# Kernel optimization log

Measured on AMD Instinct MI355X. Metric: run time of the kernel, lower is better.

The kernel has to match this reference:

```python
import jax, jax.numpy as jnp
import numpy as np

N = 100000          # num nodes
E = 1600000         # num edges (before self loops)
IN_C = 128
OUT_C = 64
RATIO = 0.5
NEG_SLOPE = 0.2


def setup_inputs() -> dict:
    key = jax.random.key(0)
    k1, k2, k3, k4, k5 = jax.random.split(key, 5)
    x = jax.random.normal(k1, (N, IN_C), jnp.float32)
    # edges with no self loops (module removes then re-adds self loops)
    src = jax.random.randint(k2, (E,), 0, N, dtype=jnp.int32)
    off = jax.random.randint(k3, (E,), 1, N, dtype=jnp.int32)
    tgt = (src + off) % N
    edge_index = jnp.stack([src, tgt])  # [2, E], row0=source(j), row1=target(i)
    # glorot init
    s_w = float(np.sqrt(6.0 / (IN_C + OUT_C)))
    weight = jax.random.uniform(k4, (IN_C, OUT_C), jnp.float32, -s_w, s_w)
    s_a = float(np.sqrt(6.0 / (1 + 2 * OUT_C)))
    att = jax.random.uniform(k5, (1, 2 * OUT_C), jnp.float32, -s_a, s_a)
    batch = jnp.zeros((N,), jnp.int32)  # single graph
    return {"x": x, "weight": weight, "att": att,
            "edge_index": edge_index, "batch": batch, "bn": 0}


def reference(x, weight, att, edge_index, batch, bn):
    # add self loops (static shapes: E + N edges)
    loops = jnp.arange(N, dtype=edge_index.dtype)
    src = jnp.concatenate([edge_index[0], loops])  # edge_index_j (source)
    tgt = jnp.concatenate([edge_index[1], loops])  # edge_index_i (target)

    h = x @ weight                      # [N, OUT_C]
    x_j = h[src]                        # [E+N, OUT_C] gathered source feats
    x_i = h[tgt]

    # alpha = (cat([x_i, x_j]) * att).sum(-1)
    alpha = x_i @ att[0, :OUT_C] + x_j @ att[0, OUT_C:]   # [E+N]
    alpha = jnp.where(alpha > 0, alpha, NEG_SLOPE * alpha)  # leaky_relu

    # edge-softmax grouped by target node (every node has a self loop -> no empty segment)
    m = jax.ops.segment_max(alpha, tgt, num_segments=N)
    a = jnp.exp(alpha - m[tgt])
    denom = jax.ops.segment_sum(a, tgt, num_segments=N)
    alpha = a / (denom[tgt] + 1e-16)

    # node importance = sum of attention over outgoing edges (grouped by source)
    alpha_sum = jax.ops.segment_sum(alpha, src, num_segments=N)

    # topk node selection (ratio of all nodes; single graph)
    k = int(np.ceil(RATIO * N))
    _, topk_idx = jax.lax.top_k(alpha_sum, k)
    node_mask = jnp.zeros((N,), bool).at[topk_idx].set(True)

    # filter_dn: keep edges whose both endpoints survive; mask instead of compacting
    edge_mask = node_mask[src] & node_mask[tgt]
    alpha_m = jnp.where(edge_mask, alpha, 0.0)

    # weighted scatter-add aggregation to target nodes (aggr='add')
    out = jax.ops.segment_sum(alpha_m[:, None] * x_j, tgt, num_segments=N)  # [N, OUT_C]
    # bn flag is 0 -> BatchNorm skipped
    return out, edge_mask, node_mask
```

## Files before the change

### kernel.cpp

```cpp
#include <hip/hip_runtime.h>
#include <stdint.h>

#define IN_C 128
#define OUT_C 64
#define NEG_SLOPE 0.2f
#define RB 256
#define RBINS 512
#define STAGE 8192
#define SCAP 5120
#define SGRID (RBINS * SCAP)
#define KC 8
#define SXW 192

typedef unsigned int u32;
typedef unsigned char u8;
typedef unsigned long long u64;

__device__ __forceinline__ u32 fenc(float f) {
  u32 u = __float_as_uint(f);
  return (u & 0x80000000u) ? ~u : (u | 0x80000000u);
}
__device__ __forceinline__ u64 key64(float v, int i) {
  return (((u64)fenc(v)) << 32) | (u64)(0xffffffffu - (u32)i);
}

__global__ __launch_bounds__(128) void k_gemm(const float* __restrict__ x,
                                              const float* __restrict__ w,
                                              const float* __restrict__ att,
                                              float* __restrict__ h,
                                              float* __restrict__ ai, float* __restrict__ aj,
                                              int N) {
  __shared__ float sw[IN_C * OUT_C];
  __shared__ float sx[KC * SXW];
  int tid = threadIdx.x;
  int rbase = blockIdx.x * 128;

  for (int i = tid; i < (IN_C * OUT_C) / 4; i += 128)
    ((float4*)sw)[i] = ((const float4*)w)[i];

  int c0 = (tid & 7) * 8;
  int rg = tid >> 3;
  int sxbase = rg * 12;
  float acc[8][8];
#pragma unroll
  for (int i = 0; i < 8; i++)
#pragma unroll
    for (int j = 0; j < 8; j++) acc[i][j] = 0.f;

  int grow = rbase + tid;
  int base = (tid >> 3) * 12 + (tid & 7);
  const float* xp = &x[(size_t)grow * IN_C];

  float4 pv0 = make_float4(0.f, 0.f, 0.f, 0.f);
  float4 pv1 = make_float4(0.f, 0.f, 0.f, 0.f);
  if (grow < N) {
    pv0 = *(const float4*)&xp[0];
    pv1 = *(const float4*)&xp[4];
  }

  for (int kb = 0; kb < IN_C; kb += KC) {
    __syncthreads();
    sx[0 * SXW + base] = pv0.x;
    sx[1 * SXW + base] = pv0.y;
    sx[2 * SXW + base] = pv0.z;
    sx[3 * SXW + base] = pv0.w;
    sx[4 * SXW + base] = pv1.x;
    sx[5 * SXW + base] = pv1.y;
    sx[6 * SXW + base] = pv1.z;
    sx[7 * SXW + base] = pv1.w;
    if (kb + KC < IN_C && grow < N) {
      pv0 = *(const float4*)&xp[kb + KC];
      pv1 = *(const float4*)&xp[kb + KC + 4];
    }
    __syncthreads();
#pragma unroll
    for (int kl = 0; kl < KC; ++kl) {
      int kg = kb + kl;
      float xr[8], wv[8];
      *(float4*)&xr[0] = *(const float4*)&sx[kl * SXW + sxbase];
      *(float4*)&xr[4] = *(const float4*)&sx[kl * SXW + sxbase + 4];
      *(float4*)&wv[0] = *(const float4*)&sw[kg * OUT_C + c0];
      *(float4*)&wv[4] = *(const float4*)&sw[kg * OUT_C + c0 + 4];
#pragma unroll
      for (int i = 0; i < 8; ++i)
#pragma unroll
        for (int j = 0; j < 8; ++j)
          acc[i][j] += xr[i] * wv[j];
    }
  }

  float pi[8], pj[8];
#pragma unroll
  for (int i = 0; i < 8; ++i) { pi[i] = 0.f; pj[i] = 0.f; }
#pragma unroll
  for (int j = 0; j < 8; ++j) {
    float a0 = att[c0 + j], a1 = att[OUT_C + c0 + j];
#pragma unroll
    for (int i = 0; i < 8; ++i) {
      pi[i] += acc[i][j] * a0;
      pj[i] += acc[i][j] * a1;
    }
  }
#pragma unroll
  for (int o = 1; o < 8; o <<= 1) {
#pragma unroll
    for (int i = 0; i < 8; ++i) {
      pi[i] += __shfl_xor(pi[i], o);
      pj[i] += __shfl_xor(pj[i], o);
    }
  }
#pragma unroll
  for (int i = 0; i < 8; ++i) {
    int row = rbase + rg * 8 + i;
    if (row < N) {
      *(float4*)&h[(size_t)row * OUT_C + c0]     = make_float4(acc[i][0], acc[i][1], acc[i][2], acc[i][3]);
      *(float4*)&h[(size_t)row * OUT_C + c0 + 4] = make_float4(acc[i][4], acc[i][5], acc[i][6], acc[i][7]);
      if ((tid & 7) == 0) { ai[row] = pi[i]; aj[row] = pj[i]; }
    }
  }
}

__global__ __launch_bounds__(256) void k_part_t(const int* __restrict__ src, const int* __restrict__ tgt,
                                                int E, int EN, int chunk,
                                                u32* __restrict__ gcurT, u32* __restrict__ bufS,
                                                u32* __restrict__ sel, u32 kSel) {
  __shared__ u32 lh[RBINS];
  __shared__ u32 cur[RBINS];
  int tid = threadIdx.x, b = blockIdx.x;
  if (b == 0 && tid == 0) { sel[0] = 0u; sel[1] = 0u; sel[2] = kSel; sel[3] = 0u; }
  for (int d = tid; d < RBINS; d += 256) lh[d] = 0u;
  __syncthreads();
  int lo = b * chunk, hi = min(lo + chunk, EN);
  for (int e = lo + tid; e < hi; e += 256) {
    int t = (e < E) ? tgt[e] : e - E;
    atomicAdd(&lh[((u32)t) >> 8], 1u);
  }
  __syncthreads();
  for (int d = tid; d < RBINS; d += 256) {
    u32 c = lh[d];
    cur[d] = c ? (u32)(d * SCAP) + atomicAdd(&gcurT[d], c) : 0u;
  }
  __syncthreads();
  for (int e = lo + tid; e < hi; e += 256) {
    int s, t;
    if (e < E) { s = src[e]; t = tgt[e]; } else { s = t = e - E; }
    u32 tb = ((u32)t) >> 8;
    u32 p = atomicAdd(&cur[tb], 1u);
    if (p < (tb + 1u) * SCAP) bufS[p] = (((u32)t & 255u) << 24) | (u32)s;
  }
}

__global__ __launch_bounds__(256) void k_rpass2(const u32* __restrict__ in, u32* __restrict__ out,
                                                const u32* __restrict__ gcurT, u32* __restrict__ gcurS,
                                                u32* __restrict__ offT,
                                                const float* __restrict__ ai, const float* __restrict__ aj,
                                                float* __restrict__ alpha,
                                                u8* __restrict__ pidx, float* __restrict__ pval,
                                                int N) {
  __shared__ u32 hist[256];
  __shared__ u32 sc[256];
  __shared__ u32 lhs[RBINS];
  __shared__ u32 stage[STAGE];
  int tid = threadIdx.x, d = blockIdx.x;
  u32 start = (u32)(d * SCAP);
  u32 cntb = min(gcurT[d], (u32)SCAP);
  u32 end = start + cntb;
  int sz = (int)cntb;
  hist[tid] = 0u;
  for (int dd = tid; dd < RBINS; dd += 256) lhs[dd] = 0u;
  __syncthreads();
  for (u32 p = start + tid; p < end; p += 256) {
    u32 it = in[p];
    atomicAdd(&hist[it >> 24], 1u);
    atomicAdd(&lhs[(it & 0xffffffu) >> 8], 1u);
  }
  __syncthreads();
  for (int dd = tid; dd < RBINS; dd += 256) {
    u32 c = lhs[dd];
    lhs[dd] = c ? (u32)(dd * SCAP) + atomicAdd(&gcurS[dd], c) : 0u;
  }
  u32 hv = hist[tid];
  sc[tid] = hv;
  __syncthreads();
  for (int o = 1; o < 256; o <<= 1) {
    u32 t = (tid >= o) ? sc[tid - o] : 0u;
    __syncthreads();
    sc[tid] += t;
    __syncthreads();
  }
  u32 excl = sc[tid] - hv;
  int node = (d << 8) + tid;
  if (node < N) offT[node] = start + excl;
  if (node == N - 1) offT[N] = start + sc[tid];
  hist[tid] = excl;
  __syncthreads();
  bool staged = (sz <= STAGE);
  for (u32 p = start + tid; p < end; p += 256) {
    u32 it = in[p];
    u32 lp = atomicAdd(&hist[it >> 24], 1u);
    if (staged) stage[lp] = it;
    else out[start + lp] = it;
  }
  __syncthreads();
  if (staged)
    for (int i = tid; i < sz; i += 256) out[start + i] = stage[i];
  __syncthreads();
  if (node < N) {
    int lb = (tid > 0) ? (int)sc[tid - 1] : 0;
    int le = (int)sc[tid];
    float an = ai[node];
    float mx = -1e30f;
    for (int i = lb; i < le; ++i) {
      u32 it = staged ? stage[i] : out[start + i];
      float a = an + aj[it & 0xffffffu];
      a = a > 0.f ? a : NEG_SLOPE * a;
      mx = fmaxf(mx, a);
      if (staged) stage[i] = __float_as_uint(a);
    }
    float sm = 0.f;
    for (int i = lb; i < le; ++i) {
      float a;
      if (staged) a = __uint_as_float(stage[i]);
      else {
        u32 it = out[start + i];
        a = an + aj[it & 0xffffffu];
        a = a > 0.f ? a : NEG_SLOPE * a;
      }
      float v = expf(a - mx);
      sm += v;
      if (staged) stage[i] = __float_as_uint(v);
      else alpha[start + i] = v;
    }
    float inv = 1.f / (sm + 1e-16f);
    for (int i = lb; i < le; ++i) {
      float v = staged ? __uint_as_float(stage[i]) : alpha[start + i];
      alpha[start + i] = v * inv;
    }
  }
  __syncthreads();
  for (u32 p = start + tid; p < end; p += 256) {
    u32 sp = out[p] & 0xffffffu;
    u32 sb = sp >> 8;
    u32 pos = atomicAdd(&lhs[sb], 1u);
    if (pos < (sb + 1u) * SCAP) {
      pidx[pos] = (u8)(sp & 255u);
      pval[pos] = alpha[p];
    }
  }
}

__global__ __launch_bounds__(256) void k_asum_acc(const u8* __restrict__ pidx,
                                                  const float* __restrict__ pval,
                                                  const u32* __restrict__ gcurS,
                                                  float* __restrict__ asum,
                                                  u32* __restrict__ hist8, u32* __restrict__ done,
                                                  u32* __restrict__ sel, int N, int nblk) {
  __shared__ float sums[256];
  __shared__ u32 lh[256];
  __shared__ u32 s[256];
  __shared__ u32 sres;
  int tid = threadIdx.x, d = blockIdx.x;
  u32 start = (u32)(d * SCAP);
  u32 end = start + min(gcurS[d], (u32)SCAP);
  sums[tid] = 0.f;
  __syncthreads();
  for (u32 p = start + tid; p < end; p += 256)
    atomicAdd(&sums[pidx[p]], pval[p]);
  __syncthreads();
  int node = d * 256 + tid;
  u32 bin = 256u;
  if (node < N) {
    float v = sums[tid];
    asum[node] = v;
    bin = (u32)(key64(v, node) >> 56) & 255u;
  }
  lh[tid] = 0u;
  __syncthreads();
  if (bin < 256u) atomicAdd(&lh[bin], 1u);
  __syncthreads();
  if (lh[tid]) atomicAdd(&hist8[tid], lh[tid]);
  __syncthreads();
  if (tid == 0)
    sres = __hip_atomic_fetch_add(&done[0], 1u, __ATOMIC_ACQ_REL, __HIP_MEMORY_SCOPE_AGENT);
  __syncthreads();
  if (sres == (u32)(nblk - 1)) {
    u32 krem = sel[2];
    u32 hv = __hip_atomic_load(&hist8[255 - tid], __ATOMIC_RELAXED, __HIP_MEMORY_SCOPE_AGENT);
    s[tid] = hv;
    __syncthreads();
    for (int o = 1; o < 256; o <<= 1) {
      u32 t = (tid >= o) ? s[tid - o] : 0u;
      __syncthreads();
      s[tid] += t;
      __syncthreads();
    }
    u32 cum = s[tid], prev = (tid > 0) ? s[tid - 1] : 0u;
    if (cum >= krem && prev < krem) {
      ((u64*)sel)[0] = (u64)(u32)(255 - tid);
      sel[2] = krem - prev;
    }
  }
}

__global__ __launch_bounds__(256) void k_histpick(const float* __restrict__ asum,
                                                  u32* __restrict__ list_out, u32* __restrict__ cnt_out,
                                                  u32* __restrict__ hist8, u32* __restrict__ done,
                                                  u32* __restrict__ sel, int N, int nblk) {
  __shared__ u32 lh[256];
  __shared__ u32 sres;
  __shared__ u32 s[256];
  int tid = threadIdx.x;
  lh[tid] = 0u;
  __syncthreads();
  u64 prefix = ((const u64*)sel)[0];
  int i = blockIdx.x * 256 + tid;
  if (i < N) {
    u64 k = key64(asum[i], i);
    if ((k >> 56) == prefix) {
      atomicAdd(&lh[(u32)(k >> 48) & 255u], 1u);
      u32 p = atomicAdd(cnt_out, 1u);
      list_out[p] = (u32)i;
    }
  }
  __syncthreads();
  if (lh[tid]) atomicAdd(&hist8[256 + tid], lh[tid]);
  __syncthreads();
  if (tid == 0)
    sres = __hip_atomic_fetch_add(&done[1], 1u, __ATOMIC_ACQ_REL, __HIP_MEMORY_SCOPE_AGENT);
  __syncthreads();
  if (sres == (u32)(nblk - 1)) {
    u32 krem = sel[2];
    u32 hv = __hip_atomic_load(&hist8[256 + (255 - tid)], __ATOMIC_RELAXED,
                               __HIP_MEMORY_SCOPE_AGENT);
    s[tid] = hv;
    __syncthreads();
    for (int o = 1; o < 256; o <<= 1) {
      u32 t = (tid >= o) ? s[tid - o] : 0u;
      __syncthreads();
      s[tid] += t;
      __syncthreads();
    }
    u32 cum = s[tid], prev = (tid > 0) ? s[tid - 1] : 0u;
    if (cum >= krem && prev < krem) {
      ((u64*)sel)[0] = (prefix << 8) | (u64)(u32)(255 - tid);
      sel[2] = krem - prev;
    }
  }
}

__global__ __launch_bounds__(256) void k_histpick_final(const float* __restrict__ asum,
                                                        const u32* __restrict__ list_in, const u32* __restrict__ cnt_in,
                                                        u32* __restrict__ list_out, u32* __restrict__ cnt_out,
                                                        u32* __restrict__ hist8, u32* __restrict__ done,
                                                        u32* __restrict__ sel, int nblk) {
  __shared__ u32 lh[256];
  __shared__ u32 s[256];
  __shared__ u32 sres;
  __shared__ u64 keys[2048];
  __shared__ u32 cc;
  __shared__ u64 sprefix;
  __shared__ u32 skrem;
  int tid = threadIdx.x;
  lh[tid] = 0u;
  __syncthreads();
  u64 prefix = ((const u64*)sel)[0];
  u32 n = *cnt_in;
  u32 i = blockIdx.x * 256 + tid;
  if (i < n) {
    int idx = (int)list_in[i];
    u64 k = key64(asum[idx], idx);
    if ((k >> 48) == prefix) {
      atomicAdd(&lh[(u32)(k >> 40) & 255u], 1u);
      u32 p = atomicAdd(cnt_out, 1u);
      list_out[p] = (u32)idx;
    }
  }
  __syncthreads();
  if (lh[tid]) atomicAdd(&hist8[512 + tid], lh[tid]);
  __syncthreads();
  if (tid == 0)
    sres = __hip_atomic_fetch_add(&done[2], 1u, __ATOMIC_ACQ_REL, __HIP_MEMORY_SCOPE_AGENT);
  __syncthreads();
  if (sres != (u32)(nblk - 1)) return;
  u32 krem = sel[2];
  u32 hv = __hip_atomic_load(&hist8[512 + (255 - tid)], __ATOMIC_RELAXED, __HIP_MEMORY_SCOPE_AGENT);
  s[tid] = hv;
  __syncthreads();
  for (int o = 1; o < 256; o <<= 1) {
    u32 t = (tid >= o) ? s[tid - o] : 0u;
    __syncthreads();
    s[tid] += t;
    __syncthreads();
  }
  {
    u32 cum = s[tid], prev = (tid > 0) ? s[tid - 1] : 0u;
    if (cum >= krem && prev < krem) { sprefix = (prefix << 8) | (u64)(u32)(255 - tid); skrem = krem - prev; }
  }
  __syncthreads();
  u64 pfx3 = sprefix;
  u32 krem3 = skrem;
  u32 n3 = *cnt_out;
  lh[tid] = 0u;
  __syncthreads();
  for (u32 j = tid; j < n3; j += 256) {
    int idx = (int)list_out[j];
    u64 k = key64(asum[idx], idx);
    if ((k >> 40) == pfx3) atomicAdd(&lh[(u32)(k >> 32) & 255u], 1u);
  }
  __syncthreads();
  s[tid] = lh[255 - tid];
  __syncthreads();
  for (int o = 1; o < 256; o <<= 1) {
    u32 t = (tid >= o) ? s[tid - o] : 0u;
    __syncthreads();
    s[tid] += t;
    __syncthreads();
  }
  {
    u32 cum = s[tid], prev = (tid > 0) ? s[tid - 1] : 0u;
    if (cum >= krem3 && prev < krem3) { sprefix = (pfx3 << 8) | (u64)(u32)(255 - tid); skrem = krem3 - prev; }
  }
  if (tid == 0) cc = 0u;
  __syncthreads();
  u32 fsel = (u32)sprefix;
  u32 kremF = skrem;
  for (u32 j = tid; j < n3; j += 256) {
    int idx = (int)list_out[j];
    u64 k = key64(asum[idx], idx);
    if ((u32)(k >> 32) == fsel) {
      u32 p = atomicAdd(&cc, 1u);
      if (p < 2048) keys[p] = k;
    }
  }
  __syncthreads();
  int C = (int)min(cc, 2048u);
  for (int j = tid; j < C; j += 256) {
    u64 k = keys[j];
    u32 rank = 0;
    for (int q = 0; q < C; ++q)
      if (keys[q] > k) rank++;
    if (rank == kremF - 1) ((u64*)sel)[0] = k;
  }
}

__global__ __launch_bounds__(256) void k_node_mask(const float* __restrict__ asum,
                                                   const u32* __restrict__ sel,
                                                   u32* __restrict__ nm,
                                                   float* __restrict__ out_node, int N) {
  int i = blockIdx.x * 256 + threadIdx.x;
  if (i >= N) return;
  u64 T = ((const u64*)sel)[0];
  bool m = key64(asum[i], i) >= T;
  nm[i] = m ? 1u : 0u;
  out_node[i] = m ? 1.f : 0.f;
}

__global__ __launch_bounds__(256) void k_mask(const int* __restrict__ src, const int* __restrict__ tgt,
                                              const u32* __restrict__ nm,
                                              const u32* __restrict__ csr, const float* __restrict__ alpha,
                                              const u32* __restrict__ gcurT,
                                              float* __restrict__ out_edge, u64* __restrict__ pair,
                                              int E, int EN) {
  int q = blockIdx.x * 256 + threadIdx.x;
  if (q < EN) {
    int s, t;
    if (q < E) { s = src[q]; t = tgt[q]; } else { s = t = q - E; }
    out_edge[q] = (nm[s] && nm[t]) ? 1.f : 0.f;
  }
  if (q < SGRID) {
    u32 b = (u32)q / (u32)SCAP;
    u32 r = (u32)q - b * (u32)SCAP;
    if (r < min(gcurT[b], (u32)SCAP)) {
      u32 sp = csr[q] & 0xffffffu;
      u32 ab = nm[sp] ? __float_as_uint(alpha[q]) : 0u;
      pair[q] = (((u64)sp) << 32) | ab;
    }
  }
}

__global__ __launch_bounds__(256) void k_aggregate(const u32* __restrict__ off,
                                                   const u64* __restrict__ pair,
                                                   const float* __restrict__ h,
                                                   const u32* __restrict__ nm,
                                                   const u32* __restrict__ gcurT,
                                                   float* __restrict__ out, int N) {
  int node = blockIdx.x * 4 + (threadIdx.x >> 6);
  int lane = threadIdx.x & 63;
  int g = lane >> 4;
  int c = lane & 15;
  if (node >= N) return;
  float4 acc = make_float4(0.f, 0.f, 0.f, 0.f);
  if (nm[node]) {
    u32 bkt = (u32)node >> 8;
    u32 bend = bkt * (u32)SCAP + min(gcurT[bkt], (u32)SCAP);
    u32 b = off[node];
    u32 e2 = min(off[node + 1], bend);
    for (u32 p0 = b; p0 < e2; p0 += 32) {
      u64 pr[8];
      float av[8];
      u32 sv[8];
#pragma unroll
      for (int q = 0; q < 8; ++q) {
        u32 p = p0 + q * 4 + (u32)g;
        bool ok = p < e2;
        pr[q] = pair[ok ? p : b];
        av[q] = ok ? __uint_as_float((u32)pr[q]) : 0.f;
        sv[q] = (u32)(pr[q] >> 32);
      }
      float4 hv[8];
#pragma unroll
      for (int q = 0; q < 8; ++q) {
        hv[q] = make_float4(0.f, 0.f, 0.f, 0.f);
        if (av[q] != 0.f)
          hv[q] = *(const float4*)&h[(size_t)sv[q] * OUT_C + c * 4];
      }
#pragma unroll
      for (int q = 0; q < 8; ++q) {
        acc.x += av[q] * hv[q].x;
        acc.y += av[q] * hv[q].y;
        acc.z += av[q] * hv[q].z;
        acc.w += av[q] * hv[q].w;
      }
    }
#pragma unroll
    for (int o = 16; o < 64; o <<= 1) {
      acc.x += __shfl_xor(acc.x, o);
      acc.y += __shfl_xor(acc.y, o);
      acc.z += __shfl_xor(acc.z, o);
      acc.w += __shfl_xor(acc.w, o);
    }
  }
  if (g == 0)
    *(float4*)&out[(size_t)node * OUT_C + c * 4] = acc;
}

extern "C" void kernel_launch(void* const* d_in, const int* in_sizes, int n_in,
                              void* d_out, int out_size, void* d_ws, size_t ws_size,
                              hipStream_t stream) {
  const float* x   = (const float*)d_in[0];
  const float* w   = (const float*)d_in[1];
  const float* att = (const float*)d_in[2];
  const int*   ei  = (const int*)d_in[3];

  int N = in_sizes[0] / IN_C;
  int E = in_sizes[3] / 2;
  int EN = E + N;
  const int* src = ei;
  const int* tgt = ei + E;

  float* out      = (float*)d_out;
  float* out_edge = out + (size_t)N * OUT_C;
  float* out_node = out_edge + (size_t)EN;

  char* p = (char*)d_ws;
  auto alloc = [&](size_t bytes) -> char* {
    char* r = p;
    p += (bytes + 255) & ~(size_t)255;
    return r;
  };
  float* h     = (float*)alloc((size_t)N * OUT_C * 4);
  float* ai    = (float*)alloc((size_t)N * 4);
  float* aj    = (float*)alloc((size_t)N * 4);
  u32*   bufA  = (u32*)alloc((size_t)SGRID * 4);
  u32*   stg   = (u32*)alloc((size_t)SGRID * 4);
  u8*    pidx  = (u8*)alloc((size_t)SGRID);
  float* pval  = (float*)alloc((size_t)SGRID * 4);
  u64*   pair  = (u64*)alloc((size_t)SGRID * 8);
  u32*   offT  = (u32*)alloc((size_t)(N + 1) * 4);
  float* asum  = (float*)alloc((size_t)N * 4);
  u32*   nm    = (u32*)alloc((size_t)N * 4);
  u32*   listA = (u32*)alloc((size_t)N * 4);
  u32*   listB = (u32*)alloc((size_t)N * 4);
  u32*   zb    = (u32*)alloc((RBINS + RBINS + 2048 + 8 + 8) * 4);
  u32*   gcurT = zb;
  u32*   gcurS = zb + RBINS;
  u32*   hist8 = zb + 2 * RBINS;
  u32*   done  = zb + 2 * RBINS + 2048;
  u32*   cnt   = zb + 2 * RBINS + 2048 + 8;
  u32*   sel   = (u32*)alloc(256);

  float* alpha = (float*)stg;

  u32 kSel = (u32)((N + 1) / 2);
  int chunk = (EN + RB - 1) / RB;
  int gGemm = (N + 127) / 128;
  int gN = (N + 255) / 256;
  int gS = (SGRID + 255) / 256;
  int gNode4 = (N + 3) / 4;

  hipMemsetAsync(zb, 0, (RBINS + RBINS + 2048 + 8 + 8) * 4, stream);

  k_gemm<<<gGemm, 128, 0, stream>>>(x, w, att, h, ai, aj, N);

  k_part_t<<<RB, 256, 0, stream>>>(src, tgt, E, EN, chunk, gcurT, stg, sel, kSel);
  k_rpass2<<<RBINS, 256, 0, stream>>>(stg, bufA, gcurT, gcurS, offT, ai, aj,
                                      alpha, pidx, pval, N);
  k_asum_acc<<<RBINS, 256, 0, stream>>>(pidx, pval, gcurS, asum, hist8, done, sel, N, RBINS);

  k_histpick<<<gN, 256, 0, stream>>>(asum, listA, &cnt[1], hist8, done, sel, N, gN);
  k_histpick_final<<<gN, 256, 0, stream>>>(asum, listA, &cnt[1], listB, &cnt[2],
                                           hist8, done, sel, gN);

  k_node_mask<<<gN, 256, 0, stream>>>(asum, sel, nm, out_node, N);
  k_mask<<<gS, 256, 0, stream>>>(src, tgt, nm, bufA, alpha, gcurT, out_edge, pair, E, EN);
  k_aggregate<<<gNode4, 256, 0, stream>>>(offT, pair, h, nm, gcurT, out, N);
}
```

Measured before the change: 329.9 us.

## Carry source attention scalar through partition buffer and stage all buckets in LDS

The partition kernel now gathers aj[src] once and packs it with the target/source word into a 64-bit entry. The radix second pass then reads that value directly instead of doing a random aj gather. Every bucket is staged in shared memory, sized to SCAP, so the global fallback path is gone and softmax values live in LDS. Source-bucket pairs are written as packed u64 (index, value) instead of separate byte and float arrays. In exchange the partition traffic is doubled to 8 bytes per entry and LDS use per block grows, which may lower occupancy.

```diff
diff --git a/kernel.cpp b/kernel.cpp
--- a/kernel.cpp
+++ b/kernel.cpp
@@ -6,7 +6,6 @@
 #define NEG_SLOPE 0.2f
 #define RB 256
 #define RBINS 512
-#define STAGE 8192
 #define SCAP 5120
 #define SGRID (RBINS * SCAP)
 #define KC 8
@@ -121,8 +120,9 @@
 }
 
 __global__ __launch_bounds__(256) void k_part_t(const int* __restrict__ src, const int* __restrict__ tgt,
+                                                const float* __restrict__ aj,
                                                 int E, int EN, int chunk,
-                                                u32* __restrict__ gcurT, u32* __restrict__ bufS,
+                                                u32* __restrict__ gcurT, u64* __restrict__ bufS,
                                                 u32* __restrict__ sel, u32 kSel) {
   __shared__ u32 lh[RBINS];
   __shared__ u32 cur[RBINS];
@@ -146,21 +146,25 @@
     if (e < E) { s = src[e]; t = tgt[e]; } else { s = t = e - E; }
     u32 tb = ((u32)t) >> 8;
     u32 p = atomicAdd(&cur[tb], 1u);
-    if (p < (tb + 1u) * SCAP) bufS[p] = (((u32)t & 255u) << 24) | (u32)s;
-  }
-}
-
-__global__ __launch_bounds__(256) void k_rpass2(const u32* __restrict__ in, u32* __restrict__ out,
+    if (p < (tb + 1u) * SCAP) {
+      float av = aj[s];
+      bufS[p] = (((u64)((((u32)t & 255u) << 24) | (u32)s)) << 32) | (u64)__float_as_uint(av);
+    }
+  }
+}
+
+__global__ __launch_bounds__(256) void k_rpass2(const u64* __restrict__ in, u32* __restrict__ out,
                                                 const u32* __restrict__ gcurT, u32* __restrict__ gcurS,
                                                 u32* __restrict__ offT,
-                                                const float* __restrict__ ai, const float* __restrict__ aj,
+                                                const float* __restrict__ ai,
                                                 float* __restrict__ alpha,
-                                                u8* __restrict__ pidx, float* __restrict__ pval,
+                                                u64* __restrict__ pv,
                                                 int N) {
   __shared__ u32 hist[256];
   __shared__ u32 sc[256];
   __shared__ u32 lhs[RBINS];
-  __shared__ u32 stage[STAGE];
+  __shared__ u32 stage[SCAP];
+  __shared__ float stageV[SCAP];
   int tid = threadIdx.x, d = blockIdx.x;
   u32 start = (u32)(d * SCAP);
   u32 cntb = min(gcurT[d], (u32)SCAP);
@@ -170,7 +174,7 @@
   for (int dd = tid; dd < RBINS; dd += 256) lhs[dd] = 0u;
   __syncthreads();
   for (u32 p = start + tid; p < end; p += 256) {
-    u32 it = in[p];
+    u32 it = (u32)(in[p] >> 32);
     atomicAdd(&hist[it >> 24], 1u);
     atomicAdd(&lhs[(it & 0xffffffu) >> 8], 1u);
   }
@@ -194,63 +198,51 @@
   if (node == N - 1) offT[N] = start + sc[tid];
   hist[tid] = excl;
   __syncthreads();
-  bool staged = (sz <= STAGE);
   for (u32 p = start + tid; p < end; p += 256) {
-    u32 it = in[p];
+    u64 it64 = in[p];
+    u32 it = (u32)(it64 >> 32);
     u32 lp = atomicAdd(&hist[it >> 24], 1u);
-    if (staged) stage[lp] = it;
-    else out[start + lp] = it;
-  }
-  __syncthreads();
-  if (staged)
-    for (int i = tid; i < sz; i += 256) out[start + i] = stage[i];
-  __syncthreads();
+    stage[lp] = it;
+    stageV[lp] = __uint_as_float((u32)it64);
+  }
+  __syncthreads();
+  for (int i = tid; i < sz; i += 256) out[start + i] = stage[i];
   if (node < N) {
     int lb = (tid > 0) ? (int)sc[tid - 1] : 0;
     int le = (int)sc[tid];
     float an = ai[node];
     float mx = -1e30f;
     for (int i = lb; i < le; ++i) {
-      u32 it = staged ? stage[i] : out[start + i];
-      float a = an + aj[it & 0xffffffu];
+      float a = an + stageV[i];
       a = a > 0.f ? a : NEG_SLOPE * a;
+      stageV[i] = a;
       mx = fmaxf(mx, a);
-      if (staged) stage[i] = __float_as_uint(a);
     }
     float sm = 0.f;
     for (int i = lb; i < le; ++i) {
-      float a;
-      if (staged) a = __uint_as_float(stage[i]);
-      else {
-        u32 it = out[start + i];
-        a = an + aj[it & 0xffffffu];
-        a = a > 0.f ? a : NEG_SLOPE * a;
-      }
-      float v = expf(a - mx);
+      float v = expf(stageV[i] - mx);
+      stageV[i] = v;
       sm += v;
-      if (staged) stage[i] = __float_as_uint(v);
-      else alpha[start + i] = v;
     }
     float inv = 1.f / (sm + 1e-16f);
     for (int i = lb; i < le; ++i) {
-      float v = staged ? __uint_as_float(stage[i]) : alpha[start + i];
-      alpha[start + i] = v * inv;
+      float vn = stageV[i] * inv;
+      stageV[i] = vn;
+      alpha[start + i] = vn;
     }
   }
   __syncthreads();
   for (u32 p = start + tid; p < end; p += 256) {
-    u32 sp = out[p] & 0xffffffu;
+    int i = (int)(p - start);
+    u32 sp = stage[i] & 0xffffffu;
     u32 sb = sp >> 8;
     u32 pos = atomicAdd(&lhs[sb], 1u);
-    if (pos < (sb + 1u) * SCAP) {
-      pidx[pos] = (u8)(sp & 255u);
-      pval[pos] = alpha[p];
-    }
-  }
-}
-
-__global__ __launch_bounds__(256) void k_asum_acc(const u8* __restrict__ pidx,
-                                                  const float* __restrict__ pval,
+    if (pos < (sb + 1u) * SCAP)
+      pv[pos] = (((u64)(sp & 255u)) << 32) | (u64)__float_as_uint(stageV[i]);
+  }
+}
+
+__global__ __launch_bounds__(256) void k_asum_acc(const u64* __restrict__ pv,
                                                   const u32* __restrict__ gcurS,
                                                   float* __restrict__ asum,
                                                   u32* __restrict__ hist8, u32* __restrict__ done,
@@ -264,8 +256,10 @@
   u32 end = start + min(gcurS[d], (u32)SCAP);
   sums[tid] = 0.f;
   __syncthreads();
-  for (u32 p = start + tid; p < end; p += 256)
-    atomicAdd(&sums[pidx[p]], pval[p]);
+  for (u32 p = start + tid; p < end; p += 256) {
+    u64 it = pv[p];
+    atomicAdd(&sums[(u32)(it >> 32)], __uint_as_float((u32)it));
+  }
   __syncthreads();
   int node = d * 256 + tid;
   u32 bin = 256u;
@@ -561,11 +555,10 @@
   float* h     = (float*)alloc((size_t)N * OUT_C * 4);
   float* ai    = (float*)alloc((size_t)N * 4);
   float* aj    = (float*)alloc((size_t)N * 4);
+  u64*   stg   = (u64*)alloc((size_t)SGRID * 8);
   u32*   bufA  = (u32*)alloc((size_t)SGRID * 4);
-  u32*   stg   = (u32*)alloc((size_t)SGRID * 4);
-  u8*    pidx  = (u8*)alloc((size_t)SGRID);
-  float* pval  = (float*)alloc((size_t)SGRID * 4);
-  u64*   pair  = (u64*)alloc((size_t)SGRID * 8);
+  float* alpha = (float*)alloc((size_t)SGRID * 4);
+  u64*   pv    = (u64*)alloc((size_t)SGRID * 8);
   u32*   offT  = (u32*)alloc((size_t)(N + 1) * 4);
   float* asum  = (float*)alloc((size_t)N * 4);
   u32*   nm    = (u32*)alloc((size_t)N * 4);
@@ -579,7 +572,7 @@
   u32*   cnt   = zb + 2 * RBINS + 2048 + 8;
   u32*   sel   = (u32*)alloc(256);
 
-  float* alpha = (float*)stg;
+  u64*   pair  = pv;
 
   u32 kSel = (u32)((N + 1) / 2);
   int chunk = (EN + RB - 1) / RB;
@@ -592,10 +585,9 @@
 
   k_gemm<<<gGemm, 128, 0, stream>>>(x, w, att, h, ai, aj, N);
 
-  k_part_t<<<RB, 256, 0, stream>>>(src, tgt, E, EN, chunk, gcurT, stg, sel, kSel);
-  k_rpass2<<<RBINS, 256, 0, stream>>>(stg, bufA, gcurT, gcurS, offT, ai, aj,
-                                      alpha, pidx, pval, N);
-  k_asum_acc<<<RBINS, 256, 0, stream>>>(pidx, pval, gcurS, asum, hist8, done, sel, N, RBINS);
+  k_part_t<<<RB, 256, 0, stream>>>(src, tgt, aj, E, EN, chunk, gcurT, stg, sel, kSel);
+  k_rpass2<<<RBINS, 256, 0, stream>>>(stg, bufA, gcurT, gcurS, offT, ai, alpha, pv, N);
+  k_asum_acc<<<RBINS, 256, 0, stream>>>(pv, gcurS, asum, hist8, done, sel, N, RBINS);
 
   k_histpick<<<gN, 256, 0, stream>>>(asum, listA, &cnt[1], hist8, done, sel, N, gN);
   k_histpick_final<<<gN, 256, 0, stream>>>(asum, listA, &cnt[1], listB, &cnt[2],
```

New measurement: 326.6 us. About the same (-1.0%).
